# Kernel optimization log

Hardware: AMD Instinct MI355X
Metric: run time of the kernel (lower is better)

## Reference

```python
import jax, jax.numpy as jnp
import numpy as np

E, H, I = 8, 2048, 4096      # experts, hidden, intermediate
T, K = 1024, 2               # tokens, top_k
GS = 128                     # quantization group size


def setup_inputs() -> dict:
    key = jax.random.key(0)
    ks = jax.random.split(key, 9)
    x = jax.random.normal(ks[0], (T, H), dtype=jnp.float32)
    # packed int4: two nibbles per uint8, [out_features, in_features // 2]
    gu_packed = jax.random.randint(ks[1], (E, 2 * I, H // 2), 0, 256, dtype=jnp.int32).astype(jnp.uint8)
    dn_packed = jax.random.randint(ks[2], (E, H, I // 2), 0, 256, dtype=jnp.int32).astype(jnp.uint8)
    # small positive scales; zeros chosen so dequantized values center near 0
    gu_scales = jax.random.uniform(ks[3], (E, 2 * I, H // GS), dtype=jnp.float32) * 0.02 + 0.001
    gu_zeros = -7.5 * gu_scales + 0.001 * jax.random.normal(ks[4], gu_scales.shape, dtype=jnp.float32)
    dn_scales = jax.random.uniform(ks[5], (E, H, I // GS), dtype=jnp.float32) * 0.02 + 0.001
    dn_zeros = -7.5 * dn_scales + 0.001 * jax.random.normal(ks[6], dn_scales.shape, dtype=jnp.float32)
    router_indices = jax.random.randint(ks[7], (T, K), 0, E, dtype=jnp.int32)
    rw = jax.random.uniform(ks[8], (T, K), dtype=jnp.float32) + 0.1
    routing_weights = rw / jnp.sum(rw, axis=-1, keepdims=True)
    return {
        "x": x,
        "gu_packed": gu_packed, "gu_scales": gu_scales, "gu_zeros": gu_zeros,
        "dn_packed": dn_packed, "dn_scales": dn_scales, "dn_zeros": dn_zeros,
        "router_indices": router_indices, "routing_weights": routing_weights,
        "group_size": GS,
    }


def _dequantize_packed_weight(packed, scales, zeros, in_features, group_size):
    """Unpack uint8 nibbles (high at even cols, low at odd cols), apply
    per-group scale and zero-point: w = q * scale + zero."""
    out_f = packed.shape[0]
    high = (packed >> 4) & 15
    low = packed & 15
    # interleave: column 0::2 = high nibble, 1::2 = low nibble
    unpacked = jnp.stack([high, low], axis=-1).reshape(out_f, -1).astype(scales.dtype)
    n_groups = scales.shape[1]
    grouped = unpacked.reshape(out_f, n_groups, group_size)
    dq = grouped * scales[:, :, None] + zeros[:, :, None]
    return dq.reshape(out_f, n_groups * group_size)[:, :in_features]


def reference(x, gu_packed, gu_scales, gu_zeros, dn_packed, dn_scales, dn_zeros,
              router_indices, routing_weights, group_size):
    num_experts = gu_packed.shape[0]
    hidden = x.shape[-1]
    inter = dn_packed.shape[2] * 2
    # per-token per-expert combine coefficient [T, E]
    one_hot = jax.nn.one_hot(router_indices, num_experts, dtype=x.dtype)  # [T, K, E]
    coef = jnp.einsum("tke,tk->te", one_hot, routing_weights)
    out = jnp.zeros_like(x)
    for e in range(num_experts):
        gu_w = _dequantize_packed_weight(gu_packed[e], gu_scales[e], gu_zeros[e], hidden, group_size)  # [2I, H]
        dn_w = _dequantize_packed_weight(dn_packed[e], dn_scales[e], dn_zeros[e], inter, group_size)   # [H, I]
        gu = x @ gu_w.T                     # [T, 2I]
        gate, up = jnp.split(gu, 2, axis=-1)
        h = jax.nn.gelu(gate, approximate=True) * up  # [T, I]
        out = out + coef[:, e:e + 1] * (h @ dn_w.T)   # [T, H]
    return out
```

## Files before the change

kernel.cpp:

```cpp
#include <hip/hip_runtime.h>
#include <hip/hip_bf16.h>
#include <stdint.h>

#define E_ 8
#define H_ 2048
#define I_ 4096
#define T_ 1024
#define K_ 2
#define GS_ 128
#define NPAIR (T_ * K_)

#define BM 64
#define BN 64
#define BK 64
#define LDK 72

typedef __attribute__((ext_vector_type(8))) short s16x8;
typedef __attribute__((ext_vector_type(4))) float f32x4;

static __device__ __forceinline__ short f2bf(float f) {
    __hip_bfloat16 h = __float2bfloat16(f);
    return __builtin_bit_cast(short, h);
}

__global__ void zero_f4(float4* p, int n4) {
    int i = blockIdx.x * blockDim.x + threadIdx.x;
    if (i < n4) p[i] = make_float4(0.f, 0.f, 0.f, 0.f);
}

__global__ void router_kernel(const int* __restrict__ ridx,
                              const float* __restrict__ rw,
                              int* __restrict__ seg,
                              int* __restrict__ ptok,
                              float* __restrict__ pw)
{
    __shared__ int cnt[E_];
    __shared__ int cur[E_];
    int tid = threadIdx.x;
    if (tid < E_) cnt[tid] = 0;
    __syncthreads();
    for (int p = tid; p < NPAIR; p += blockDim.x)
        atomicAdd(&cnt[ridx[p]], 1);
    __syncthreads();
    if (tid == 0) {
        int s = 0;
        for (int e = 0; e < E_; e++) { seg[e] = s; cur[e] = s; s += cnt[e]; }
        seg[E_] = s;
    }
    __syncthreads();
    for (int p = tid; p < NPAIR; p += blockDim.x) {
        int e = ridx[p];
        int pos = atomicAdd(&cur[e], 1);
        ptok[pos] = p >> 1;
        pw[pos] = rw[p];
    }
}

static __device__ __forceinline__ void dq16(const int* __restrict__ prow,
                                            int koff_bytes, float sc, float zp,
                                            short* tw) {
    int4 pa = *(const int4*)(prow + koff_bytes);
    int4 pb = *(const int4*)(prow + koff_bytes + 4);
    int q[8] = {pa.x, pa.y, pa.z, pa.w, pb.x, pb.y, pb.z, pb.w};
#pragma unroll
    for (int j = 0; j < 8; j++) {
        uint32_t byte = (uint32_t)q[j] & 0xffu;
        tw[2 * j]     = f2bf((float)(byte >> 4) * sc + zp);
        tw[2 * j + 1] = f2bf((float)(byte & 15u) * sc + zp);
    }
}

__global__ __launch_bounds__(256) void gemm1_kernel(
    const float* __restrict__ x,
    const int* __restrict__ gu_packed,
    const float* __restrict__ gu_scales,
    const float* __restrict__ gu_zeros,
    const int* __restrict__ seg,
    const int* __restrict__ ptok,
    unsigned short* __restrict__ h_act)
{
    const int e = blockIdx.z;
    const int seg0 = seg[e], seg1 = seg[e + 1];
    const int m0 = blockIdx.y * BM;
    if (seg0 + m0 >= seg1) return;
    const int n0 = blockIdx.x * BN;

    __shared__ short sX[BM][LDK];
    __shared__ short sG[BN][LDK];
    __shared__ short sU[BN][LDK];

    const int tid = threadIdx.x;
    const int lane = tid & 63;
    const int wave = tid >> 6;
    const int wm = (wave & 1) * 32;
    const int wn = (wave >> 1) * 32;
    const int quad = lane >> 4;
    const int l16 = lane & 15;

    const int srow = tid >> 2;
    const int scol = (tid & 3) * 16;

    int slotS = seg0 + m0 + srow;
    if (slotS > NPAIR - 1) slotS = NPAIR - 1;
    const int tok = ptok[slotS];
    const float* xrow = x + (size_t)tok * H_;

    const int ng = n0 + srow;
    const int nu = n0 + I_ + srow;
    const int* gprow = gu_packed + ((size_t)e * (2 * I_) + ng) * (H_ / 2) + (tid & 3) * 8;
    const int* uprow = gu_packed + ((size_t)e * (2 * I_) + nu) * (H_ / 2) + (tid & 3) * 8;
    const float* gsrow = gu_scales + ((size_t)e * (2 * I_) + ng) * (H_ / GS_);
    const float* gzrow = gu_zeros  + ((size_t)e * (2 * I_) + ng) * (H_ / GS_);
    const float* usrow = gu_scales + ((size_t)e * (2 * I_) + nu) * (H_ / GS_);
    const float* uzrow = gu_zeros  + ((size_t)e * (2 * I_) + nu) * (H_ / GS_);

    f32x4 accg[2][2], accu[2][2];
#pragma unroll
    for (int mi = 0; mi < 2; mi++)
#pragma unroll
        for (int ni = 0; ni < 2; ni++) {
            accg[mi][ni] = (f32x4){0.f, 0.f, 0.f, 0.f};
            accu[mi][ni] = (f32x4){0.f, 0.f, 0.f, 0.f};
        }

    for (int k0 = 0; k0 < H_; k0 += BK) {
        {
            const float4* xp = (const float4*)(xrow + k0 + scol);
            short tx[16];
#pragma unroll
            for (int q = 0; q < 4; q++) {
                float4 f = xp[q];
                tx[4 * q + 0] = f2bf(f.x);
                tx[4 * q + 1] = f2bf(f.y);
                tx[4 * q + 2] = f2bf(f.z);
                tx[4 * q + 3] = f2bf(f.w);
            }
            *(s16x8*)&sX[srow][scol]     = *(s16x8*)&tx[0];
            *(s16x8*)&sX[srow][scol + 8] = *(s16x8*)&tx[8];
        }
        const int g = k0 >> 7;
        {
            short tw[16];
            dq16(gprow, k0 >> 1, gsrow[g], gzrow[g], tw);
            *(s16x8*)&sG[srow][scol]     = *(s16x8*)&tw[0];
            *(s16x8*)&sG[srow][scol + 8] = *(s16x8*)&tw[8];
        }
        {
            short tw[16];
            dq16(uprow, k0 >> 1, usrow[g], uzrow[g], tw);
            *(s16x8*)&sU[srow][scol]     = *(s16x8*)&tw[0];
            *(s16x8*)&sU[srow][scol + 8] = *(s16x8*)&tw[8];
        }
        __syncthreads();

#pragma unroll
        for (int ks = 0; ks < BK; ks += 32) {
            s16x8 af[2], gf[2], uf[2];
#pragma unroll
            for (int i = 0; i < 2; i++) {
                af[i] = *(const s16x8*)&sX[wm + i * 16 + l16][ks + quad * 8];
                gf[i] = *(const s16x8*)&sG[wn + i * 16 + l16][ks + quad * 8];
                uf[i] = *(const s16x8*)&sU[wn + i * 16 + l16][ks + quad * 8];
            }
#pragma unroll
            for (int mi = 0; mi < 2; mi++)
#pragma unroll
                for (int ni = 0; ni < 2; ni++) {
                    accg[mi][ni] = __builtin_amdgcn_mfma_f32_16x16x32_bf16(af[mi], gf[ni], accg[mi][ni], 0, 0, 0);
                    accu[mi][ni] = __builtin_amdgcn_mfma_f32_16x16x32_bf16(af[mi], uf[ni], accu[mi][ni], 0, 0, 0);
                }
        }
        __syncthreads();
    }

#pragma unroll
    for (int mi = 0; mi < 2; mi++) {
#pragma unroll
        for (int r = 0; r < 4; r++) {
            const int row = wm + mi * 16 + quad * 4 + r;
            const int slot = seg0 + m0 + row;
            if (slot < seg1) {
#pragma unroll
                for (int ni = 0; ni < 2; ni++) {
                    const int col = n0 + wn + ni * 16 + l16;
                    float gv = accg[mi][ni][r];
                    float uv = accu[mi][ni][r];
                    float t = tanhf(0.7978845608028654f * (gv + 0.044715f * gv * gv * gv));
                    float hv = 0.5f * gv * (1.0f + t) * uv;
                    h_act[(size_t)slot * I_ + col] = (unsigned short)f2bf(hv);
                }
            }
        }
    }
}

__global__ __launch_bounds__(256) void gemm2_kernel(
    const unsigned short* __restrict__ h_act,
    const int* __restrict__ dn_packed,
    const float* __restrict__ dn_scales,
    const float* __restrict__ dn_zeros,
    const int* __restrict__ seg,
    const int* __restrict__ ptok,
    const float* __restrict__ pw,
    float* __restrict__ out)
{
    const int e = blockIdx.z;
    const int seg0 = seg[e], seg1 = seg[e + 1];
    const int m0 = blockIdx.y * BM;
    if (seg0 + m0 >= seg1) return;
    const int n0 = blockIdx.x * BN;

    __shared__ short sA[BM][LDK];
    __shared__ short sW[BN][LDK];

    const int tid = threadIdx.x;
    const int lane = tid & 63;
    const int wave = tid >> 6;
    const int wm = (wave & 1) * 32;
    const int wn = (wave >> 1) * 32;
    const int quad = lane >> 4;
    const int l16 = lane & 15;

    const int srow = tid >> 2;
    const int scol = (tid & 3) * 16;

    int slotS = seg0 + m0 + srow;
    if (slotS > NPAIR - 1) slotS = NPAIR - 1;
    const unsigned short* hrow = h_act + (size_t)slotS * I_;

    const int nw = n0 + srow;
    const int* wprow = dn_packed + ((size_t)e * H_ + nw) * (I_ / 2) + (tid & 3) * 8;
    const float* wsrow = dn_scales + ((size_t)e * H_ + nw) * (I_ / GS_);
    const float* wzrow = dn_zeros  + ((size_t)e * H_ + nw) * (I_ / GS_);

    f32x4 acc[2][2];
#pragma unroll
    for (int mi = 0; mi < 2; mi++)
#pragma unroll
        for (int ni = 0; ni < 2; ni++)
            acc[mi][ni] = (f32x4){0.f, 0.f, 0.f, 0.f};

    for (int k0 = 0; k0 < I_; k0 += BK) {
        {
            const s16x8* hp = (const s16x8*)(hrow + k0 + scol);
            *(s16x8*)&sA[srow][scol]     = hp[0];
            *(s16x8*)&sA[srow][scol + 8] = hp[1];
        }
        {
            const int g = k0 >> 7;
            short tw[16];
            dq16(wprow, k0 >> 1, wsrow[g], wzrow[g], tw);
            *(s16x8*)&sW[srow][scol]     = *(s16x8*)&tw[0];
            *(s16x8*)&sW[srow][scol + 8] = *(s16x8*)&tw[8];
        }
        __syncthreads();

#pragma unroll
        for (int ks = 0; ks < BK; ks += 32) {
            s16x8 af[2], wf[2];
#pragma unroll
            for (int i = 0; i < 2; i++) {
                af[i] = *(const s16x8*)&sA[wm + i * 16 + l16][ks + quad * 8];
                wf[i] = *(const s16x8*)&sW[wn + i * 16 + l16][ks + quad * 8];
            }
#pragma unroll
            for (int mi = 0; mi < 2; mi++)
#pragma unroll
                for (int ni = 0; ni < 2; ni++)
                    acc[mi][ni] = __builtin_amdgcn_mfma_f32_16x16x32_bf16(af[mi], wf[ni], acc[mi][ni], 0, 0, 0);
        }
        __syncthreads();
    }

#pragma unroll
    for (int mi = 0; mi < 2; mi++) {
#pragma unroll
        for (int r = 0; r < 4; r++) {
            const int row = wm + mi * 16 + quad * 4 + r;
            const int slot = seg0 + m0 + row;
            if (slot < seg1) {
                const int tok = ptok[slot];
                const float cf = pw[slot];
#pragma unroll
                for (int ni = 0; ni < 2; ni++) {
                    const int col = n0 + wn + ni * 16 + l16;
                    atomicAdd(&out[(size_t)tok * H_ + col], cf * acc[mi][ni][r]);
                }
            }
        }
    }
}

extern "C" void kernel_launch(void* const* d_in, const int* in_sizes, int n_in,
                              void* d_out, int out_size, void* d_ws, size_t ws_size,
                              hipStream_t stream) {
    const float* x    = (const float*)d_in[0];
    const int*   gu_p = (const int*)d_in[1];
    const float* gu_s = (const float*)d_in[2];
    const float* gu_z = (const float*)d_in[3];
    const int*   dn_p = (const int*)d_in[4];
    const float* dn_s = (const float*)d_in[5];
    const float* dn_z = (const float*)d_in[6];
    const int*   ridx = (const int*)d_in[7];
    const float* rw   = (const float*)d_in[8];

    char* ws = (char*)d_ws;
    int*            seg   = (int*)ws;
    int*            ptok  = (int*)(ws + 256);
    float*          pw    = (float*)(ws + 256 + NPAIR * 4);
    unsigned short* h_act = (unsigned short*)(ws + 32768);

    float* out = (float*)d_out;

    zero_f4<<<(T_ * H_ / 4 + 255) / 256, 256, 0, stream>>>((float4*)out, T_ * H_ / 4);
    router_kernel<<<1, 256, 0, stream>>>(ridx, rw, seg, ptok, pw);
    gemm1_kernel<<<dim3(I_ / BN, NPAIR / BM, E_), 256, 0, stream>>>(
        x, gu_p, gu_s, gu_z, seg, ptok, h_act);
    gemm2_kernel<<<dim3(H_ / BN, NPAIR / BM, E_), 256, 0, stream>>>(
        h_act, dn_p, dn_s, dn_z, seg, ptok, pw, out);
}
```

Before: 797.4 us.

## Enlarge M tile, prefetch to registers, swizzle LDS, preconvert x to bf16

Doubles the M tile to 128 so each dequantized weight tile is reused across more tokens, cutting redundant int4 dequant and weight loads per expert. Adds register prefetch of the next K-slice while MFMAs run, an XOR-swizzled LDS layout in place of padding, a cheaper packed bf16 conversion, and a separate pre-pass that converts x to bf16 once. These raise register pressure (launch bounds of 3 blocks) and add an extra kernel launch plus workspace buffer.

```diff
diff --git a/kernel.cpp b/kernel.cpp
--- a/kernel.cpp
+++ b/kernel.cpp
@@ -10,17 +10,33 @@
 #define GS_ 128
 #define NPAIR (T_ * K_)
 
-#define BM 64
+#define BM 128
 #define BN 64
 #define BK 64
-#define LDK 72
+
+#define CH(r, c) ((((c) ^ ((r) & 7)) << 3))
 
 typedef __attribute__((ext_vector_type(8))) short s16x8;
 typedef __attribute__((ext_vector_type(4))) float f32x4;
 
-static __device__ __forceinline__ short f2bf(float f) {
+static __device__ __forceinline__ unsigned short f2bf(float f) {
     __hip_bfloat16 h = __float2bfloat16(f);
-    return __builtin_bit_cast(short, h);
+    return __builtin_bit_cast(unsigned short, h);
+}
+static __device__ __forceinline__ uint32_t pk2(float lo16, float hi16) {
+    uint32_t a = __builtin_bit_cast(uint32_t, lo16) + 0x8000u;
+    uint32_t b = __builtin_bit_cast(uint32_t, hi16) + 0x8000u;
+    return (a >> 16) | (b & 0xffff0000u);
+}
+
+__global__ void x2bf_kernel(const float* __restrict__ x, unsigned short* __restrict__ xb) {
+    int i = (blockIdx.x * 256 + threadIdx.x) * 8;
+    float4 a = *(const float4*)(x + i);
+    float4 b = *(const float4*)(x + i + 4);
+    unsigned short t[8];
+    t[0] = f2bf(a.x); t[1] = f2bf(a.y); t[2] = f2bf(a.z); t[3] = f2bf(a.w);
+    t[4] = f2bf(b.x); t[5] = f2bf(b.y); t[6] = f2bf(b.z); t[7] = f2bf(b.w);
+    *(s16x8*)(xb + i) = *(s16x8*)t;
 }
 
 __global__ void zero_f4(float4* p, int n4) {
@@ -56,22 +72,22 @@
     }
 }
 
-static __device__ __forceinline__ void dq16(const int* __restrict__ prow,
-                                            int koff_bytes, float sc, float zp,
-                                            short* tw) {
-    int4 pa = *(const int4*)(prow + koff_bytes);
-    int4 pb = *(const int4*)(prow + koff_bytes + 4);
-    int q[8] = {pa.x, pa.y, pa.z, pa.w, pb.x, pb.y, pb.z, pb.w};
-#pragma unroll
-    for (int j = 0; j < 8; j++) {
-        uint32_t byte = (uint32_t)q[j] & 0xffu;
-        tw[2 * j]     = f2bf((float)(byte >> 4) * sc + zp);
-        tw[2 * j + 1] = f2bf((float)(byte & 15u) * sc + zp);
-    }
-}
-
-__global__ __launch_bounds__(256) void gemm1_kernel(
-    const float* __restrict__ x,
+static __device__ __forceinline__ void dq_chunk(int4 q, float sc, float zp,
+                                                unsigned short* dst) {
+    uint32_t r[4];
+    int qa[4] = {q.x, q.y, q.z, q.w};
+#pragma unroll
+    for (int j = 0; j < 4; j++) {
+        uint32_t byte = (uint32_t)qa[j] & 0xffu;
+        float fh = (float)(byte >> 4) * sc + zp;
+        float fl = (float)(byte & 15u) * sc + zp;
+        r[j] = pk2(fh, fl);
+    }
+    *(uint4*)dst = make_uint4(r[0], r[1], r[2], r[3]);
+}
+
+__global__ __launch_bounds__(256, 3) void gemm1_kernel(
+    const unsigned short* __restrict__ xb,
     const int* __restrict__ gu_packed,
     const float* __restrict__ gu_scales,
     const float* __restrict__ gu_zeros,
@@ -85,28 +101,28 @@
     if (seg0 + m0 >= seg1) return;
     const int n0 = blockIdx.x * BN;
 
-    __shared__ short sX[BM][LDK];
-    __shared__ short sG[BN][LDK];
-    __shared__ short sU[BN][LDK];
+    __shared__ __align__(16) unsigned short sX[BM * 64];
+    __shared__ __align__(16) unsigned short sG[BN * 64];
+    __shared__ __align__(16) unsigned short sU[BN * 64];
 
     const int tid = threadIdx.x;
     const int lane = tid & 63;
     const int wave = tid >> 6;
-    const int wm = (wave & 1) * 32;
-    const int wn = (wave >> 1) * 32;
+    const int wm = (wave >> 1) * 64;
+    const int wn = (wave & 1) * 32;
     const int quad = lane >> 4;
     const int l16 = lane & 15;
 
-    const int srow = tid >> 2;
-    const int scol = (tid & 3) * 16;
-
-    int slotS = seg0 + m0 + srow;
-    if (slotS > NPAIR - 1) slotS = NPAIR - 1;
-    const int tok = ptok[slotS];
-    const float* xrow = x + (size_t)tok * H_;
-
-    const int ng = n0 + srow;
-    const int nu = n0 + I_ + srow;
+    const int xr = tid >> 1;
+    const int xc0 = (tid & 1) * 4;
+    int slotX = seg0 + m0 + xr;
+    if (slotX > NPAIR - 1) slotX = NPAIR - 1;
+    const unsigned short* xrow = xb + (size_t)ptok[slotX] * H_ + xc0 * 8;
+
+    const int wr = tid >> 2;
+    const int wc0 = (tid & 3) * 2;
+    const int ng = n0 + wr;
+    const int nu = n0 + I_ + wr;
     const int* gprow = gu_packed + ((size_t)e * (2 * I_) + ng) * (H_ / 2) + (tid & 3) * 8;
     const int* uprow = gu_packed + ((size_t)e * (2 * I_) + nu) * (H_ / 2) + (tid & 3) * 8;
     const float* gsrow = gu_scales + ((size_t)e * (2 * I_) + ng) * (H_ / GS_);
@@ -114,56 +130,69 @@
     const float* usrow = gu_scales + ((size_t)e * (2 * I_) + nu) * (H_ / GS_);
     const float* uzrow = gu_zeros  + ((size_t)e * (2 * I_) + nu) * (H_ / GS_);
 
-    f32x4 accg[2][2], accu[2][2];
-#pragma unroll
-    for (int mi = 0; mi < 2; mi++)
+    f32x4 accg[4][2], accu[4][2];
+#pragma unroll
+    for (int mi = 0; mi < 4; mi++)
 #pragma unroll
         for (int ni = 0; ni < 2; ni++) {
             accg[mi][ni] = (f32x4){0.f, 0.f, 0.f, 0.f};
             accu[mi][ni] = (f32x4){0.f, 0.f, 0.f, 0.f};
         }
 
+    s16x8 rX[4];
+    int4 rG[2], rU[2];
+    float rgs, rgz, rus, ruz;
+
+    {
+        const s16x8* xp = (const s16x8*)(xrow);
+        rX[0] = xp[0]; rX[1] = xp[1]; rX[2] = xp[2]; rX[3] = xp[3];
+        const int4* gp = (const int4*)(gprow);
+        rG[0] = gp[0]; rG[1] = gp[1];
+        const int4* up = (const int4*)(uprow);
+        rU[0] = up[0]; rU[1] = up[1];
+        rgs = gsrow[0]; rgz = gzrow[0]; rus = usrow[0]; ruz = uzrow[0];
+    }
+
     for (int k0 = 0; k0 < H_; k0 += BK) {
-        {
-            const float4* xp = (const float4*)(xrow + k0 + scol);
-            short tx[16];
-#pragma unroll
-            for (int q = 0; q < 4; q++) {
-                float4 f = xp[q];
-                tx[4 * q + 0] = f2bf(f.x);
-                tx[4 * q + 1] = f2bf(f.y);
-                tx[4 * q + 2] = f2bf(f.z);
-                tx[4 * q + 3] = f2bf(f.w);
-            }
-            *(s16x8*)&sX[srow][scol]     = *(s16x8*)&tx[0];
-            *(s16x8*)&sX[srow][scol + 8] = *(s16x8*)&tx[8];
-        }
-        const int g = k0 >> 7;
-        {
-            short tw[16];
-            dq16(gprow, k0 >> 1, gsrow[g], gzrow[g], tw);
-            *(s16x8*)&sG[srow][scol]     = *(s16x8*)&tw[0];
-            *(s16x8*)&sG[srow][scol + 8] = *(s16x8*)&tw[8];
-        }
-        {
-            short tw[16];
-            dq16(uprow, k0 >> 1, usrow[g], uzrow[g], tw);
-            *(s16x8*)&sU[srow][scol]     = *(s16x8*)&tw[0];
-            *(s16x8*)&sU[srow][scol + 8] = *(s16x8*)&tw[8];
-        }
+        *(s16x8*)&sX[(xr << 6) + CH(xr, xc0 + 0)] = rX[0];
+        *(s16x8*)&sX[(xr << 6) + CH(xr, xc0 + 1)] = rX[1];
+        *(s16x8*)&sX[(xr << 6) + CH(xr, xc0 + 2)] = rX[2];
+        *(s16x8*)&sX[(xr << 6) + CH(xr, xc0 + 3)] = rX[3];
+        dq_chunk(rG[0], rgs, rgz, &sG[(wr << 6) + CH(wr, wc0)]);
+        dq_chunk(rG[1], rgs, rgz, &sG[(wr << 6) + CH(wr, wc0 + 1)]);
+        dq_chunk(rU[0], rus, ruz, &sU[(wr << 6) + CH(wr, wc0)]);
+        dq_chunk(rU[1], rus, ruz, &sU[(wr << 6) + CH(wr, wc0 + 1)]);
         __syncthreads();
 
-#pragma unroll
-        for (int ks = 0; ks < BK; ks += 32) {
-            s16x8 af[2], gf[2], uf[2];
+        if (k0 + BK < H_) {
+            const int k1 = k0 + BK;
+            const s16x8* xp = (const s16x8*)(xrow + k1);
+            rX[0] = xp[0]; rX[1] = xp[1]; rX[2] = xp[2]; rX[3] = xp[3];
+            const int4* gp = (const int4*)(gprow + (k1 >> 1));
+            rG[0] = gp[0]; rG[1] = gp[1];
+            const int4* up = (const int4*)(uprow + (k1 >> 1));
+            rU[0] = up[0]; rU[1] = up[1];
+            const int g = k1 >> 7;
+            rgs = gsrow[g]; rgz = gzrow[g]; rus = usrow[g]; ruz = uzrow[g];
+        }
+
+#pragma unroll
+        for (int ks = 0; ks < 2; ks++) {
+            const int cb = ks * 4 + quad;
+            s16x8 af[4], gf[2], uf[2];
+#pragma unroll
+            for (int i = 0; i < 4; i++) {
+                const int r = wm + i * 16 + l16;
+                af[i] = *(const s16x8*)&sX[(r << 6) + CH(r, cb)];
+            }
 #pragma unroll
             for (int i = 0; i < 2; i++) {
-                af[i] = *(const s16x8*)&sX[wm + i * 16 + l16][ks + quad * 8];
-                gf[i] = *(const s16x8*)&sG[wn + i * 16 + l16][ks + quad * 8];
-                uf[i] = *(const s16x8*)&sU[wn + i * 16 + l16][ks + quad * 8];
-            }
-#pragma unroll
-            for (int mi = 0; mi < 2; mi++)
+                const int r = wn + i * 16 + l16;
+                gf[i] = *(const s16x8*)&sG[(r << 6) + CH(r, cb)];
+                uf[i] = *(const s16x8*)&sU[(r << 6) + CH(r, cb)];
+            }
+#pragma unroll
+            for (int mi = 0; mi < 4; mi++)
 #pragma unroll
                 for (int ni = 0; ni < 2; ni++) {
                     accg[mi][ni] = __builtin_amdgcn_mfma_f32_16x16x32_bf16(af[mi], gf[ni], accg[mi][ni], 0, 0, 0);
@@ -174,27 +203,27 @@
     }
 
 #pragma unroll
-    for (int mi = 0; mi < 2; mi++) {
-#pragma unroll
-        for (int r = 0; r < 4; r++) {
-            const int row = wm + mi * 16 + quad * 4 + r;
+    for (int mi = 0; mi < 4; mi++) {
+#pragma unroll
+        for (int rr = 0; rr < 4; rr++) {
+            const int row = wm + mi * 16 + quad * 4 + rr;
             const int slot = seg0 + m0 + row;
             if (slot < seg1) {
 #pragma unroll
                 for (int ni = 0; ni < 2; ni++) {
                     const int col = n0 + wn + ni * 16 + l16;
-                    float gv = accg[mi][ni][r];
-                    float uv = accu[mi][ni][r];
+                    float gv = accg[mi][ni][rr];
+                    float uv = accu[mi][ni][rr];
                     float t = tanhf(0.7978845608028654f * (gv + 0.044715f * gv * gv * gv));
                     float hv = 0.5f * gv * (1.0f + t) * uv;
-                    h_act[(size_t)slot * I_ + col] = (unsigned short)f2bf(hv);
+                    h_act[(size_t)slot * I_ + col] = f2bf(hv);
                 }
             }
         }
     }
 }
 
-__global__ __launch_bounds__(256) void gemm2_kernel(
+__global__ __launch_bounds__(256, 3) void gemm2_kernel(
     const unsigned short* __restrict__ h_act,
     const int* __restrict__ dn_packed,
     const float* __restrict__ dn_scales,
@@ -210,61 +239,84 @@
     if (seg0 + m0 >= seg1) return;
     const int n0 = blockIdx.x * BN;
 
-    __shared__ short sA[BM][LDK];
-    __shared__ short sW[BN][LDK];
+    __shared__ __align__(16) unsigned short sA[BM * 64];
+    __shared__ __align__(16) unsigned short sW[BN * 64];
 
     const int tid = threadIdx.x;
     const int lane = tid & 63;
     const int wave = tid >> 6;
-    const int wm = (wave & 1) * 32;
-    const int wn = (wave >> 1) * 32;
+    const int wm = (wave >> 1) * 64;
+    const int wn = (wave & 1) * 32;
     const int quad = lane >> 4;
     const int l16 = lane & 15;
 
-    const int srow = tid >> 2;
-    const int scol = (tid & 3) * 16;
-
-    int slotS = seg0 + m0 + srow;
-    if (slotS > NPAIR - 1) slotS = NPAIR - 1;
-    const unsigned short* hrow = h_act + (size_t)slotS * I_;
-
-    const int nw = n0 + srow;
+    const int ar = tid >> 1;
+    const int ac0 = (tid & 1) * 4;
+    int slotA = seg0 + m0 + ar;
+    if (slotA > NPAIR - 1) slotA = NPAIR - 1;
+    const unsigned short* arow = h_act + (size_t)slotA * I_ + ac0 * 8;
+
+    const int wr = tid >> 2;
+    const int wc0 = (tid & 3) * 2;
+    const int nw = n0 + wr;
     const int* wprow = dn_packed + ((size_t)e * H_ + nw) * (I_ / 2) + (tid & 3) * 8;
     const float* wsrow = dn_scales + ((size_t)e * H_ + nw) * (I_ / GS_);
     const float* wzrow = dn_zeros  + ((size_t)e * H_ + nw) * (I_ / GS_);
 
-    f32x4 acc[2][2];
-#pragma unroll
-    for (int mi = 0; mi < 2; mi++)
+    f32x4 acc[4][2];
+#pragma unroll
+    for (int mi = 0; mi < 4; mi++)
 #pragma unroll
         for (int ni = 0; ni < 2; ni++)
             acc[mi][ni] = (f32x4){0.f, 0.f, 0.f, 0.f};
 
+    s16x8 rA[4];
+    int4 rW[2];
+    float rs, rz;
+
+    {
+        const s16x8* ap = (const s16x8*)(arow);
+        rA[0] = ap[0]; rA[1] = ap[1]; rA[2] = ap[2]; rA[3] = ap[3];
+        const int4* wp = (const int4*)(wprow);
+        rW[0] = wp[0]; rW[1] = wp[1];
+        rs = wsrow[0]; rz = wzrow[0];
+    }
+
     for (int k0 = 0; k0 < I_; k0 += BK) {
-        {
-            const s16x8* hp = (const s16x8*)(hrow + k0 + scol);
-            *(s16x8*)&sA[srow][scol]     = hp[0];
-            *(s16x8*)&sA[srow][scol + 8] = hp[1];
-        }
-        {
-            const int g = k0 >> 7;
-            short tw[16];
-            dq16(wprow, k0 >> 1, wsrow[g], wzrow[g], tw);
-            *(s16x8*)&sW[srow][scol]     = *(s16x8*)&tw[0];
-            *(s16x8*)&sW[srow][scol + 8] = *(s16x8*)&tw[8];
-        }
+        *(s16x8*)&sA[(ar << 6) + CH(ar, ac0 + 0)] = rA[0];
+        *(s16x8*)&sA[(ar << 6) + CH(ar, ac0 + 1)] = rA[1];
+        *(s16x8*)&sA[(ar << 6) + CH(ar, ac0 + 2)] = rA[2];
+        *(s16x8*)&sA[(ar << 6) + CH(ar, ac0 + 3)] = rA[3];
+        dq_chunk(rW[0], rs, rz, &sW[(wr << 6) + CH(wr, wc0)]);
+        dq_chunk(rW[1], rs, rz, &sW[(wr << 6) + CH(wr, wc0 + 1)]);
         __syncthreads();
 
-#pragma unroll
-        for (int ks = 0; ks < BK; ks += 32) {
-            s16x8 af[2], wf[2];
+        if (k0 + BK < I_) {
+            const int k1 = k0 + BK;
+            const s16x8* ap = (const s16x8*)(arow + k1);
+            rA[0] = ap[0]; rA[1] = ap[1]; rA[2] = ap[2]; rA[3] = ap[3];
+            const int4* wp = (const int4*)(wprow + (k1 >> 1));
+            rW[0] = wp[0]; rW[1] = wp[1];
+            const int g = k1 >> 7;
+            rs = wsrow[g]; rz = wzrow[g];
+        }
+
+#pragma unroll
+        for (int ks = 0; ks < 2; ks++) {
+            const int cb = ks * 4 + quad;
+            s16x8 af[4], wf[2];
+#pragma unroll
+            for (int i = 0; i < 4; i++) {
+                const int r = wm + i * 16 + l16;
+                af[i] = *(const s16x8*)&sA[(r << 6) + CH(r, cb)];
+            }
 #pragma unroll
             for (int i = 0; i < 2; i++) {
-                af[i] = *(const s16x8*)&sA[wm + i * 16 + l16][ks + quad * 8];
-                wf[i] = *(const s16x8*)&sW[wn + i * 16 + l16][ks + quad * 8];
-            }
-#pragma unroll
-            for (int mi = 0; mi < 2; mi++)
+                const int r = wn + i * 16 + l16;
+                wf[i] = *(const s16x8*)&sW[(r << 6) + CH(r, cb)];
+            }
+#pragma unroll
+            for (int mi = 0; mi < 4; mi++)
 #pragma unroll
                 for (int ni = 0; ni < 2; ni++)
                     acc[mi][ni] = __builtin_amdgcn_mfma_f32_16x16x32_bf16(af[mi], wf[ni], acc[mi][ni], 0, 0, 0);
@@ -273,10 +325,10 @@
     }
 
 #pragma unroll
-    for (int mi = 0; mi < 2; mi++) {
-#pragma unroll
-        for (int r = 0; r < 4; r++) {
-            const int row = wm + mi * 16 + quad * 4 + r;
+    for (int mi = 0; mi < 4; mi++) {
+#pragma unroll
+        for (int rr = 0; rr < 4; rr++) {
+            const int row = wm + mi * 16 + quad * 4 + rr;
             const int slot = seg0 + m0 + row;
             if (slot < seg1) {
                 const int tok = ptok[slot];
@@ -284,7 +336,7 @@
 #pragma unroll
                 for (int ni = 0; ni < 2; ni++) {
                     const int col = n0 + wn + ni * 16 + l16;
-                    atomicAdd(&out[(size_t)tok * H_ + col], cf * acc[mi][ni][r]);
+                    atomicAdd(&out[(size_t)tok * H_ + col], cf * acc[mi][ni][rr]);
                 }
             }
         }
@@ -309,13 +361,15 @@
     int*            ptok  = (int*)(ws + 256);
     float*          pw    = (float*)(ws + 256 + NPAIR * 4);
     unsigned short* h_act = (unsigned short*)(ws + 32768);
+    unsigned short* xb    = (unsigned short*)(ws + 32768 + (size_t)NPAIR * I_ * 2);
 
     float* out = (float*)d_out;
 
+    x2bf_kernel<<<T_ * H_ / (256 * 8), 256, 0, stream>>>(x, xb);
     zero_f4<<<(T_ * H_ / 4 + 255) / 256, 256, 0, stream>>>((float4*)out, T_ * H_ / 4);
     router_kernel<<<1, 256, 0, stream>>>(ridx, rw, seg, ptok, pw);
     gemm1_kernel<<<dim3(I_ / BN, NPAIR / BM, E_), 256, 0, stream>>>(
-        x, gu_p, gu_s, gu_z, seg, ptok, h_act);
+        xb, gu_p, gu_s, gu_z, seg, ptok, h_act);
     gemm2_kernel<<<dim3(H_ / BN, NPAIR / BM, E_), 256, 0, stream>>>(
         h_act, dn_p, dn_s, dn_z, seg, ptok, pw, out);
 }
```

Result: faster. 691.5 us (-13.3%).
